# Kernel tuning notes

Hardware: AMD Instinct MI355X
Metric: run time of the kernel (lower is better)

The kernel has to match this reference:

```python
import jax, jax.numpy as jnp
import numpy as np

MARGIN = 1.0  # from init_kwargs


def _cdist(a, b):
    # Euclidean pairwise distances, [N, D] x [M, D] -> [N, M]
    sq = (jnp.sum(a * a, axis=1)[:, None]
          + jnp.sum(b * b, axis=1)[None, :]
          - 2.0 * (a @ b.T))
    return jnp.sqrt(jnp.maximum(sq, 0.0))


def setup_inputs() -> dict:
    key = jax.random.key(0)
    k1, k2 = jax.random.split(key)
    N, D = 8192, 128
    return {
        "output1": jax.random.normal(k1, (N, D), dtype=jnp.float32),
        "output2": jax.random.normal(k2, (N, D), dtype=jnp.float32),
    }


def reference(output1, output2):
    d = _cdist(output1, output2)  # [N, M]
    N, M = d.shape

    # image -> text direction (loop over rows i in the original)
    jmin = jnp.argmin(d, axis=1)            # [N] positive index per row
    pos_r = jnp.min(d, axis=1)              # [N] pos_distance = d[i, jmin[i]]
    hinge_r = jnp.maximum(0.0, MARGIN - pos_r[:, None] + d)  # [N, M]
    # exclude the positive (argmin) column from each row's mean
    hinge_r = jnp.where(jnp.arange(M)[None, :] == jmin[:, None], 0.0, hinge_r)
    image_losses = hinge_r.mean(axis=1)     # [N]

    # text -> image direction (loop over columns i in the original)
    imin = jnp.argmin(d, axis=0)            # [M]
    pos_c = jnp.min(d, axis=0)              # [M]
    hinge_c = jnp.maximum(0.0, MARGIN - pos_c[None, :] + d)  # [N, M]
    hinge_c = jnp.where(jnp.arange(N)[:, None] == imin[None, :], 0.0, hinge_c)
    text_losses = hinge_c.mean(axis=0)      # [M]

    return (image_losses.mean() + text_losses.mean()) * 0.5
```

## Files before the change

kernel.cpp:

```cpp
#include <hip/hip_runtime.h>
#include <hip/hip_bf16.h>
#include <math.h>

#define NN 8192
#define DD 128
#define BIGF 3.402823466e+38f

typedef __attribute__((ext_vector_type(8))) short short8;
typedef __attribute__((ext_vector_type(4))) float f32x4;

static __device__ __forceinline__ unsigned short bfc(float f) {
    return __bfloat16_as_ushort(__float2bfloat16(f));
}

__global__ __launch_bounds__(256) void prep_kernel(const float* __restrict__ A,
                                                   const float* __restrict__ B,
                                                   __hip_bfloat16* __restrict__ Abf,
                                                   __hip_bfloat16* __restrict__ Bbf,
                                                   float* __restrict__ na,
                                                   float* __restrict__ nb) {
    const float* x = blockIdx.y ? B : A;
    __hip_bfloat16* xb = blockIdx.y ? Bbf : Abf;
    float* norm = blockIdx.y ? nb : na;
    const int sub = threadIdx.x >> 5;
    const int ch  = threadIdx.x & 31;
    const int row = blockIdx.x * 8 + sub;
    const float4 v = *(const float4*)(x + (size_t)row * DD + ch * 4);
    float s = v.x * v.x + v.y * v.y + v.z * v.z + v.w * v.w;
    uint2 pk;
    pk.x = ((unsigned)bfc(v.y) << 16) | bfc(v.x);
    pk.y = ((unsigned)bfc(v.w) << 16) | bfc(v.z);
    *(uint2*)(xb + (size_t)row * DD + ch * 4) = pk;
#pragma unroll
    for (int off = 16; off >= 1; off >>= 1) s += __shfl_xor(s, off, 64);
    if (ch == 0) norm[row] = s;
}

__global__ __launch_bounds__(256, 4) void dist_fused(
    const __hip_bfloat16* __restrict__ Ab, const __hip_bfloat16* __restrict__ Bb,
    const float* __restrict__ na, const float* __restrict__ nb,
    float* __restrict__ rowpart, float* __restrict__ colpart,
    float* __restrict__ totpart) {
    __shared__ char lds[32768];
    char* ldsA = lds;
    char* ldsB = lds + 16384;
    const int tid = threadIdx.x;
    const int rowBase = blockIdx.y * 128;
    const int colBase = blockIdx.x * 128;

    const unsigned short* aG = (const unsigned short*)Ab + (size_t)rowBase * DD;
    const unsigned short* bG = (const unsigned short*)Bb + (size_t)colBase * DD;

    const int l = tid & 63, wid = tid >> 6;
    const int wr = wid >> 1, wc = wid & 1;
    const int g = l >> 4, c = l & 15;

    f32x4 acc[4][4];
#pragma unroll
    for (int mi = 0; mi < 4; ++mi)
#pragma unroll
        for (int ni = 0; ni < 4; ++ni) acc[mi][ni] = (f32x4)0.f;

#pragma unroll
    for (int p = 0; p < 2; ++p) {
        if (p) __syncthreads();
#pragma unroll
        for (int it = 0; it < 4; ++it) {
            int idx = tid + 256 * it;
            int r = idx >> 3;
            int c16 = idx & 7;
            int dst = r * 128 + ((c16 * 16) ^ ((r & 7) << 4));
            *(short8*)(ldsA + dst) = *(const short8*)(aG + r * DD + p * 64 + c16 * 8);
            *(short8*)(ldsB + dst) = *(const short8*)(bG + r * DD + p * 64 + c16 * 8);
        }
        __syncthreads();
#pragma unroll
        for (int kk = 0; kk < 2; ++kk) {
            short8 af[4], bf[4];
            const int kbyte = kk * 64 + g * 16;
#pragma unroll
            for (int mi = 0; mi < 4; ++mi) {
                int r = wr * 64 + mi * 16 + c;
                af[mi] = *(const short8*)(ldsA + r * 128 + (kbyte ^ ((r & 7) << 4)));
                int r2 = wc * 64 + mi * 16 + c;
                bf[mi] = *(const short8*)(ldsB + r2 * 128 + (kbyte ^ ((r2 & 7) << 4)));
            }
#pragma unroll
            for (int mi = 0; mi < 4; ++mi)
#pragma unroll
                for (int ni = 0; ni < 4; ++ni)
                    acc[mi][ni] = __builtin_amdgcn_mfma_f32_16x16x32_bf16(
                        af[mi], bf[ni], acc[mi][ni], 0, 0, 0);
        }
    }

    const int row0 = rowBase + wr * 64;
    const int col0 = colBase + wc * 64;

    float nbc[4];
#pragma unroll
    for (int ni = 0; ni < 4; ++ni) nbc[ni] = nb[col0 + ni * 16 + c];

    float* rmbuf = (float*)lds;
    float* cmbuf = (float*)(lds + 1024);
    float* tbuf  = (float*)(lds + 2048);
    __syncthreads();

    float colm2[4] = {BIGF, BIGF, BIGF, BIGF};
    f32x4 tot4 = (f32x4)0.f;
#pragma unroll
    for (int mi = 0; mi < 4; ++mi) {
        const f32x4 na4 = *(const f32x4*)(na + row0 + mi * 16 + g * 4);
        float rowm2[4] = {BIGF, BIGF, BIGF, BIGF};
#pragma unroll
        for (int ni = 0; ni < 4; ++ni) {
            f32x4 a = acc[mi][ni];
#pragma unroll
            for (int reg = 0; reg < 4; ++reg) {
                float d2 = fmaf(-2.0f, a[reg], na4[reg] + nbc[ni]);
                rowm2[reg] = fminf(rowm2[reg], d2);
                colm2[ni] = fminf(colm2[ni], d2);
                tot4[reg] += __builtin_amdgcn_sqrtf(fmaxf(d2, 0.f));
            }
        }
#pragma unroll
        for (int reg = 0; reg < 4; ++reg) {
            float m = rowm2[reg];
            m = fminf(m, __shfl_xor(m, 1, 64));
            m = fminf(m, __shfl_xor(m, 2, 64));
            m = fminf(m, __shfl_xor(m, 4, 64));
            m = fminf(m, __shfl_xor(m, 8, 64));
            if (c == 0) rmbuf[wc * 128 + wr * 64 + mi * 16 + g * 4 + reg] = m;
        }
    }
#pragma unroll
    for (int ni = 0; ni < 4; ++ni) {
        float m = colm2[ni];
        m = fminf(m, __shfl_xor(m, 16, 64));
        m = fminf(m, __shfl_xor(m, 32, 64));
        if (g == 0) cmbuf[wr * 128 + wc * 64 + ni * 16 + c] = m;
    }
    float tot = (tot4[0] + tot4[1]) + (tot4[2] + tot4[3]);
#pragma unroll
    for (int off = 32; off >= 1; off >>= 1) tot += __shfl_xor(tot, off, 64);
    if (l == 0) tbuf[wid] = tot;
    __syncthreads();

    if (tid < 128) {
        rowpart[(size_t)blockIdx.x * NN + rowBase + tid] =
            fminf(rmbuf[tid], rmbuf[128 + tid]);
    } else if (tid < 256) {
        int j = tid - 128;
        colpart[(size_t)blockIdx.y * NN + colBase + j] =
            fminf(cmbuf[j], cmbuf[128 + j]);
    }
    if (tid == 0)
        totpart[blockIdx.y * 64 + blockIdx.x] = tbuf[0] + tbuf[1] + tbuf[2] + tbuf[3];
}

__global__ __launch_bounds__(256) void fin1_kernel(const float* __restrict__ rowpart,
                                                   const float* __restrict__ colpart,
                                                   const float* __restrict__ totpart,
                                                   float* __restrict__ finpart) {
    const int idx = blockIdx.x * 256 + threadIdx.x;
    const int j = (idx < NN) ? idx : idx - NN;
    const float* p = (idx < NN) ? rowpart : colpart;
    float m = BIGF;
#pragma unroll 8
    for (int k = 0; k < 64; ++k) m = fminf(m, p[(size_t)k * NN + j]);
    float contrib = -__builtin_amdgcn_sqrtf(fmaxf(m, 0.f)) * (1.0f / 16384.0f);
    if (blockIdx.x < 16)
        contrib += totpart[blockIdx.x * 256 + threadIdx.x] * (1.0f / 67108864.0f);
#pragma unroll
    for (int off = 32; off >= 1; off >>= 1) contrib += __shfl_xor(contrib, off, 64);
    __shared__ float red[4];
    if ((threadIdx.x & 63) == 0) red[threadIdx.x >> 6] = contrib;
    __syncthreads();
    if (threadIdx.x == 0)
        finpart[blockIdx.x] = red[0] + red[1] + red[2] + red[3];
}

__global__ __launch_bounds__(64) void fin2_kernel(const float* __restrict__ finpart,
                                                  float* __restrict__ out) {
    float s = finpart[threadIdx.x];
#pragma unroll
    for (int off = 32; off >= 1; off >>= 1) s += __shfl_xor(s, off, 64);
    if (threadIdx.x == 0) out[0] = s + 1.0f - 1.0f / 8192.0f;
}

extern "C" void kernel_launch(void* const* d_in, const int* in_sizes, int n_in,
                              void* d_out, int out_size, void* d_ws, size_t ws_size,
                              hipStream_t stream) {
    const float* A = (const float*)d_in[0];
    const float* B = (const float*)d_in[1];
    char* ws = (char*)d_ws;

    const size_t MB = 1024 * 1024;
    __hip_bfloat16* Abf = (__hip_bfloat16*)(ws);
    __hip_bfloat16* Bbf = (__hip_bfloat16*)(ws + 2 * MB);
    float* na      = (float*)(ws + 4 * MB);
    float* nb      = (float*)(ws + 4 * MB + 32768);
    float* rowpart = (float*)(ws + 4 * MB + 65536);
    float* colpart = (float*)(ws + 6 * MB + 65536);
    float* totpart = (float*)(ws + 8 * MB + 65536);
    float* finpart = (float*)(ws + 8 * MB + 65536 + 16384);

    dim3 pgrid(NN / 8, 2);
    prep_kernel<<<pgrid, 256, 0, stream>>>(A, B, Abf, Bbf, na, nb);

    dim3 grid(NN / 128, NN / 128);
    dist_fused<<<grid, 256, 0, stream>>>(Abf, Bbf, na, nb, rowpart, colpart, totpart);

    fin1_kernel<<<64, 256, 0, stream>>>(rowpart, colpart, totpart, finpart);
    fin2_kernel<<<1, 64, 0, stream>>>(finpart, (float*)d_out);
}
```

Measured before the change: 67.33 us.

## Fuse final reduction kernels via atomic counter and swizzle block order

Merges the two final reduction kernels into one, using an atomic done-counter so the last block sums the partials, which removes a kernel launch. Remaps the tile grid with an XCD-aware swizzle (groups of 8 consecutive block IDs spread across 512-strided tiles) to improve L2 locality of A/B tiles. Moves the epilogue scratch buffers out of the shared GEMM buffer so one __syncthreads can be dropped, at the cost of slightly more LDS per block.

```diff
diff --git a/kernel.cpp b/kernel.cpp
--- a/kernel.cpp
+++ b/kernel.cpp
@@ -18,7 +18,9 @@
                                                    __hip_bfloat16* __restrict__ Abf,
                                                    __hip_bfloat16* __restrict__ Bbf,
                                                    float* __restrict__ na,
-                                                   float* __restrict__ nb) {
+                                                   float* __restrict__ nb,
+                                                   unsigned int* __restrict__ done) {
+    if (blockIdx.y == 0 && blockIdx.x == 0 && threadIdx.x == 0) *done = 0u;
     const float* x = blockIdx.y ? B : A;
     __hip_bfloat16* xb = blockIdx.y ? Bbf : Abf;
     float* norm = blockIdx.y ? nb : na;
@@ -42,11 +44,18 @@
     float* __restrict__ rowpart, float* __restrict__ colpart,
     float* __restrict__ totpart) {
     __shared__ char lds[32768];
+    __shared__ float rmbuf[2][128];
+    __shared__ float cmbuf[2][128];
+    __shared__ float tbuf[4];
     char* ldsA = lds;
     char* ldsB = lds + 16384;
     const int tid = threadIdx.x;
-    const int rowBase = blockIdx.y * 128;
-    const int colBase = blockIdx.x * 128;
+
+    const int lin = blockIdx.y * 64 + blockIdx.x;
+    const int swz = (lin & 7) * 512 + (lin >> 3);
+    const int bx = swz & 63, by = swz >> 6;
+    const int rowBase = by * 128;
+    const int colBase = bx * 128;
 
     const unsigned short* aG = (const unsigned short*)Ab + (size_t)rowBase * DD;
     const unsigned short* bG = (const unsigned short*)Bb + (size_t)colBase * DD;
@@ -101,11 +110,6 @@
 #pragma unroll
     for (int ni = 0; ni < 4; ++ni) nbc[ni] = nb[col0 + ni * 16 + c];
 
-    float* rmbuf = (float*)lds;
-    float* cmbuf = (float*)(lds + 1024);
-    float* tbuf  = (float*)(lds + 2048);
-    __syncthreads();
-
     float colm2[4] = {BIGF, BIGF, BIGF, BIGF};
     f32x4 tot4 = (f32x4)0.f;
 #pragma unroll
@@ -130,7 +134,7 @@
             m = fminf(m, __shfl_xor(m, 2, 64));
             m = fminf(m, __shfl_xor(m, 4, 64));
             m = fminf(m, __shfl_xor(m, 8, 64));
-            if (c == 0) rmbuf[wc * 128 + wr * 64 + mi * 16 + g * 4 + reg] = m;
+            if (c == 0) rmbuf[wc][wr * 64 + mi * 16 + g * 4 + reg] = m;
         }
     }
 #pragma unroll
@@ -138,7 +142,7 @@
         float m = colm2[ni];
         m = fminf(m, __shfl_xor(m, 16, 64));
         m = fminf(m, __shfl_xor(m, 32, 64));
-        if (g == 0) cmbuf[wr * 128 + wc * 64 + ni * 16 + c] = m;
+        if (g == 0) cmbuf[wr][wc * 64 + ni * 16 + c] = m;
     }
     float tot = (tot4[0] + tot4[1]) + (tot4[2] + tot4[3]);
 #pragma unroll
@@ -147,21 +151,21 @@
     __syncthreads();
 
     if (tid < 128) {
-        rowpart[(size_t)blockIdx.x * NN + rowBase + tid] =
-            fminf(rmbuf[tid], rmbuf[128 + tid]);
+        rowpart[(size_t)bx * NN + rowBase + tid] = fminf(rmbuf[0][tid], rmbuf[1][tid]);
     } else if (tid < 256) {
         int j = tid - 128;
-        colpart[(size_t)blockIdx.y * NN + colBase + j] =
-            fminf(cmbuf[j], cmbuf[128 + j]);
+        colpart[(size_t)by * NN + colBase + j] = fminf(cmbuf[0][j], cmbuf[1][j]);
     }
     if (tid == 0)
-        totpart[blockIdx.y * 64 + blockIdx.x] = tbuf[0] + tbuf[1] + tbuf[2] + tbuf[3];
-}
-
-__global__ __launch_bounds__(256) void fin1_kernel(const float* __restrict__ rowpart,
-                                                   const float* __restrict__ colpart,
-                                                   const float* __restrict__ totpart,
-                                                   float* __restrict__ finpart) {
+        totpart[by * 64 + bx] = tbuf[0] + tbuf[1] + tbuf[2] + tbuf[3];
+}
+
+__global__ __launch_bounds__(256) void fin_kernel(const float* __restrict__ rowpart,
+                                                  const float* __restrict__ colpart,
+                                                  const float* __restrict__ totpart,
+                                                  float* __restrict__ finpart,
+                                                  unsigned int* __restrict__ done,
+                                                  float* __restrict__ out) {
     const int idx = blockIdx.x * 256 + threadIdx.x;
     const int j = (idx < NN) ? idx : idx - NN;
     const float* p = (idx < NN) ? rowpart : colpart;
@@ -174,18 +178,23 @@
 #pragma unroll
     for (int off = 32; off >= 1; off >>= 1) contrib += __shfl_xor(contrib, off, 64);
     __shared__ float red[4];
+    __shared__ unsigned last;
     if ((threadIdx.x & 63) == 0) red[threadIdx.x >> 6] = contrib;
     __syncthreads();
-    if (threadIdx.x == 0)
+    if (threadIdx.x == 0) {
         finpart[blockIdx.x] = red[0] + red[1] + red[2] + red[3];
-}
-
-__global__ __launch_bounds__(64) void fin2_kernel(const float* __restrict__ finpart,
-                                                  float* __restrict__ out) {
-    float s = finpart[threadIdx.x];
-#pragma unroll
-    for (int off = 32; off >= 1; off >>= 1) s += __shfl_xor(s, off, 64);
-    if (threadIdx.x == 0) out[0] = s + 1.0f - 1.0f / 8192.0f;
+        __threadfence();
+        last = (atomicAdd(done, 1u) == 63u) ? 1u : 0u;
+    }
+    __syncthreads();
+    if (last && threadIdx.x < 64) {
+        __threadfence();
+        float s = __hip_atomic_load(&finpart[threadIdx.x], __ATOMIC_RELAXED,
+                                    __HIP_MEMORY_SCOPE_AGENT);
+#pragma unroll
+        for (int off = 32; off >= 1; off >>= 1) s += __shfl_xor(s, off, 64);
+        if (threadIdx.x == 0) out[0] = s + 1.0f - 1.0f / 8192.0f;
+    }
 }
 
 extern "C" void kernel_launch(void* const* d_in, const int* in_sizes, int n_in,
@@ -204,13 +213,14 @@
     float* colpart = (float*)(ws + 6 * MB + 65536);
     float* totpart = (float*)(ws + 8 * MB + 65536);
     float* finpart = (float*)(ws + 8 * MB + 65536 + 16384);
+    unsigned int* done = (unsigned int*)(ws + 8 * MB + 65536 + 16384 + 256);
 
     dim3 pgrid(NN / 8, 2);
-    prep_kernel<<<pgrid, 256, 0, stream>>>(A, B, Abf, Bbf, na, nb);
+    prep_kernel<<<pgrid, 256, 0, stream>>>(A, B, Abf, Bbf, na, nb, done);
 
     dim3 grid(NN / 128, NN / 128);
     dist_fused<<<grid, 256, 0, stream>>>(Abf, Bbf, na, nb, rowpart, colpart, totpart);
 
-    fin1_kernel<<<64, 256, 0, stream>>>(rowpart, colpart, totpart, finpart);
-    fin2_kernel<<<1, 64, 0, stream>>>(finpart, (float*)d_out);
-}
+    fin_kernel<<<64, 256, 0, stream>>>(rowpart, colpart, totpart, finpart, done,
+                                       (float*)d_out);
+}
```

Measured after the change: 66.72 us. No clear change (-0.9%).

## Pre-swizzle bf16 operands into MFMA fragment layout and load directly from global

Applied to the files above, without the earlier changes.

The prep kernel now writes the bf16 copies of both inputs in a layout that matches the MFMA 16x16x32 operand fragments, so each lane can load its short8 fragment straight from global memory. This removes the LDS staging of A and B tiles and its __syncthreads. A block-index swizzle is added to improve L2 reuse, and launch bounds drop to 2 blocks per CU. Each wave now loads its fragments independently, so tiles shared between waves are fetched twice through cache instead of once into LDS.

```diff
diff --git a/kernel.cpp b/kernel.cpp
--- a/kernel.cpp
+++ b/kernel.cpp
@@ -15,12 +15,12 @@
 
 __global__ __launch_bounds__(256) void prep_kernel(const float* __restrict__ A,
                                                    const float* __restrict__ B,
-                                                   __hip_bfloat16* __restrict__ Abf,
-                                                   __hip_bfloat16* __restrict__ Bbf,
+                                                   char* __restrict__ Af,
+                                                   char* __restrict__ Bf,
                                                    float* __restrict__ na,
                                                    float* __restrict__ nb) {
     const float* x = blockIdx.y ? B : A;
-    __hip_bfloat16* xb = blockIdx.y ? Bbf : Abf;
+    char* xf = blockIdx.y ? Bf : Af;
     float* norm = blockIdx.y ? nb : na;
     const int sub = threadIdx.x >> 5;
     const int ch  = threadIdx.x & 31;
@@ -30,30 +30,35 @@
     uint2 pk;
     pk.x = ((unsigned)bfc(v.y) << 16) | bfc(v.x);
     pk.y = ((unsigned)bfc(v.w) << 16) | bfc(v.z);
-    *(uint2*)(xb + (size_t)row * DD + ch * 4) = pk;
+    const int rt = row >> 4, c = row & 15;
+    const int kk = ch >> 3, g = (ch >> 1) & 3, e0 = (ch & 1) * 4;
+    *(uint2*)(xf + (size_t)(rt * 4 + kk) * 1024 + g * 256 + c * 16 + e0 * 2) = pk;
 #pragma unroll
     for (int off = 16; off >= 1; off >>= 1) s += __shfl_xor(s, off, 64);
     if (ch == 0) norm[row] = s;
 }
 
-__global__ __launch_bounds__(256, 4) void dist_fused(
-    const __hip_bfloat16* __restrict__ Ab, const __hip_bfloat16* __restrict__ Bb,
+__global__ __launch_bounds__(256, 2) void dist_fused(
+    const char* __restrict__ Af, const char* __restrict__ Bf,
     const float* __restrict__ na, const float* __restrict__ nb,
     float* __restrict__ rowpart, float* __restrict__ colpart,
     float* __restrict__ totpart) {
-    __shared__ char lds[32768];
-    char* ldsA = lds;
-    char* ldsB = lds + 16384;
+    __shared__ float rmbuf[2][128];
+    __shared__ float cmbuf[2][128];
+    __shared__ float tbuf[4];
     const int tid = threadIdx.x;
-    const int rowBase = blockIdx.y * 128;
-    const int colBase = blockIdx.x * 128;
-
-    const unsigned short* aG = (const unsigned short*)Ab + (size_t)rowBase * DD;
-    const unsigned short* bG = (const unsigned short*)Bb + (size_t)colBase * DD;
-
     const int l = tid & 63, wid = tid >> 6;
     const int wr = wid >> 1, wc = wid & 1;
     const int g = l >> 4, c = l & 15;
+
+    const int lin = blockIdx.y * 64 + blockIdx.x;
+    const int swz = (lin & 7) * 512 + (lin >> 3);
+    const int bx = swz & 63, by = swz >> 6;
+    const int rowBase = by * 128;
+    const int colBase = bx * 128;
+
+    const char* aF = Af + (size_t)(by * 8 + wr * 4) * 4096 + l * 16;
+    const char* bF = Bf + (size_t)(bx * 8 + wc * 4) * 4096 + l * 16;
 
     f32x4 acc[4][4];
 #pragma unroll
@@ -62,36 +67,20 @@
         for (int ni = 0; ni < 4; ++ni) acc[mi][ni] = (f32x4)0.f;
 
 #pragma unroll
-    for (int p = 0; p < 2; ++p) {
-        if (p) __syncthreads();
+    for (int kk = 0; kk < 4; ++kk) {
+        short8 af[4], bf[4];
 #pragma unroll
-        for (int it = 0; it < 4; ++it) {
-            int idx = tid + 256 * it;
-            int r = idx >> 3;
-            int c16 = idx & 7;
-            int dst = r * 128 + ((c16 * 16) ^ ((r & 7) << 4));
-            *(short8*)(ldsA + dst) = *(const short8*)(aG + r * DD + p * 64 + c16 * 8);
-            *(short8*)(ldsB + dst) = *(const short8*)(bG + r * DD + p * 64 + c16 * 8);
-        }
-        __syncthreads();
+        for (int mi = 0; mi < 4; ++mi)
+            af[mi] = *(const short8*)(aF + mi * 4096 + kk * 1024);
 #pragma unroll
-        for (int kk = 0; kk < 2; ++kk) {
-            short8 af[4], bf[4];
-            const int kbyte = kk * 64 + g * 16;
+        for (int ni = 0; ni < 4; ++ni)
+            bf[ni] = *(const short8*)(bF + ni * 4096 + kk * 1024);
 #pragma unroll
-            for (int mi = 0; mi < 4; ++mi) {
-                int r = wr * 64 + mi * 16 + c;
-                af[mi] = *(const short8*)(ldsA + r * 128 + (kbyte ^ ((r & 7) << 4)));
-                int r2 = wc * 64 + mi * 16 + c;
-                bf[mi] = *(const short8*)(ldsB + r2 * 128 + (kbyte ^ ((r2 & 7) << 4)));
-            }
+        for (int mi = 0; mi < 4; ++mi)
 #pragma unroll
-            for (int mi = 0; mi < 4; ++mi)
-#pragma unroll
-                for (int ni = 0; ni < 4; ++ni)
-                    acc[mi][ni] = __builtin_amdgcn_mfma_f32_16x16x32_bf16(
-                        af[mi], bf[ni], acc[mi][ni], 0, 0, 0);
-        }
+            for (int ni = 0; ni < 4; ++ni)
+                acc[mi][ni] = __builtin_amdgcn_mfma_f32_16x16x32_bf16(
+                    af[mi], bf[ni], acc[mi][ni], 0, 0, 0);
     }
 
     const int row0 = rowBase + wr * 64;
@@ -100,11 +89,6 @@
     float nbc[4];
 #pragma unroll
     for (int ni = 0; ni < 4; ++ni) nbc[ni] = nb[col0 + ni * 16 + c];
-
-    float* rmbuf = (float*)lds;
-    float* cmbuf = (float*)(lds + 1024);
-    float* tbuf  = (float*)(lds + 2048);
-    __syncthreads();
 
     float colm2[4] = {BIGF, BIGF, BIGF, BIGF};
     f32x4 tot4 = (f32x4)0.f;
@@ -130,7 +114,7 @@
             m = fminf(m, __shfl_xor(m, 2, 64));
             m = fminf(m, __shfl_xor(m, 4, 64));
             m = fminf(m, __shfl_xor(m, 8, 64));
-            if (c == 0) rmbuf[wc * 128 + wr * 64 + mi * 16 + g * 4 + reg] = m;
+            if (c == 0) rmbuf[wc][wr * 64 + mi * 16 + g * 4 + reg] = m;
         }
     }
 #pragma unroll
@@ -138,7 +122,7 @@
         float m = colm2[ni];
         m = fminf(m, __shfl_xor(m, 16, 64));
         m = fminf(m, __shfl_xor(m, 32, 64));
-        if (g == 0) cmbuf[wr * 128 + wc * 64 + ni * 16 + c] = m;
+        if (g == 0) cmbuf[wr][wc * 64 + ni * 16 + c] = m;
     }
     float tot = (tot4[0] + tot4[1]) + (tot4[2] + tot4[3]);
 #pragma unroll
@@ -147,15 +131,13 @@
     __syncthreads();
 
     if (tid < 128) {
-        rowpart[(size_t)blockIdx.x * NN + rowBase + tid] =
-            fminf(rmbuf[tid], rmbuf[128 + tid]);
+        rowpart[(size_t)bx * NN + rowBase + tid] = fminf(rmbuf[0][tid], rmbuf[1][tid]);
     } else if (tid < 256) {
         int j = tid - 128;
-        colpart[(size_t)blockIdx.y * NN + colBase + j] =
-            fminf(cmbuf[j], cmbuf[128 + j]);
+        colpart[(size_t)by * NN + colBase + j] = fminf(cmbuf[0][j], cmbuf[1][j]);
     }
     if (tid == 0)
-        totpart[blockIdx.y * 64 + blockIdx.x] = tbuf[0] + tbuf[1] + tbuf[2] + tbuf[3];
+        totpart[by * 64 + bx] = tbuf[0] + tbuf[1] + tbuf[2] + tbuf[3];
 }
 
 __global__ __launch_bounds__(256) void fin1_kernel(const float* __restrict__ rowpart,
@@ -196,8 +178,8 @@
     char* ws = (char*)d_ws;
 
     const size_t MB = 1024 * 1024;
-    __hip_bfloat16* Abf = (__hip_bfloat16*)(ws);
-    __hip_bfloat16* Bbf = (__hip_bfloat16*)(ws + 2 * MB);
+    char* Af       = ws;
+    char* Bf       = ws + 2 * MB;
     float* na      = (float*)(ws + 4 * MB);
     float* nb      = (float*)(ws + 4 * MB + 32768);
     float* rowpart = (float*)(ws + 4 * MB + 65536);
@@ -206,10 +188,10 @@
     float* finpart = (float*)(ws + 8 * MB + 65536 + 16384);
 
     dim3 pgrid(NN / 8, 2);
-    prep_kernel<<<pgrid, 256, 0, stream>>>(A, B, Abf, Bbf, na, nb);
+    prep_kernel<<<pgrid, 256, 0, stream>>>(A, B, Af, Bf, na, nb);
 
     dim3 grid(NN / 128, NN / 128);
-    dist_fused<<<grid, 256, 0, stream>>>(Abf, Bbf, na, nb, rowpart, colpart, totpart);
+    dist_fused<<<grid, 256, 0, stream>>>(Af, Bf, na, nb, rowpart, colpart, totpart);
 
     fin1_kernel<<<64, 256, 0, stream>>>(rowpart, colpart, totpart, finpart);
     fin2_kernel<<<1, 64, 0, stream>>>(finpart, (float*)d_out);
```

Result: no change. 67.69 us (+0.5%).
